# Kernel tuning notes

Measured on AMD Instinct MI355X. Metric: run time of the kernel, lower is better.

Reference implementation:

```python
import jax, jax.numpy as jnp
import numpy as np

EPS = 1e-12  # torch F.normalize eps

def _l2n(x, axis):
    n = jnp.linalg.norm(x, axis=axis, keepdims=True)
    return x / jnp.maximum(n, EPS)

def setup_inputs() -> dict:
    key = jax.random.key(0)
    ks = jax.random.split(key, 11)
    B, N, D = 8, 4096, 512
    s = 1.0 / np.sqrt(D)
    return {
        'a': jax.random.normal(ks[0], (B, N, D), jnp.float32),
        'b': jax.random.normal(ks[1], (B, N, D), jnp.float32),
        'Wq': jax.random.normal(ks[2], (D, D), jnp.float32) * s,
        'bq': jax.random.normal(ks[3], (D,), jnp.float32) * s,
        'Wk': jax.random.normal(ks[4], (D, D), jnp.float32) * s,
        'bk': jax.random.normal(ks[5], (D,), jnp.float32) * s,
        'w_g': jax.random.normal(ks[6], (D, 1), jnp.float32),
        'Wp': jax.random.normal(ks[7], (D, D), jnp.float32) * s,
        'bp': jax.random.normal(ks[8], (D,), jnp.float32) * s,
        'Wf': jax.random.normal(ks[9], (D, D), jnp.float32) * s,
        'bf': jax.random.normal(ks[10], (D,), jnp.float32) * s,
    }

def reference(a, b, Wq, bq, Wk, bk, w_g, Wp, bp, Wf, bf):
    D = a.shape[-1]
    scale = D ** (-0.5)
    query = _l2n(jnp.einsum('bnd,ed->bne', a, Wq) + bq, axis=-1)   # [B,N,D]
    key = _l2n(jnp.einsum('bnd,ed->bne', b, Wk) + bk, axis=-1)     # [B,N,D]
    A = (query @ w_g) * scale                                      # [B,N,1]
    A = _l2n(A, axis=1)                                            # normalize over seq
    G = jnp.sum(A * query, axis=1)                                 # [B,D] learned pooling
    gk = G[:, None, :] * key                                       # broadcast [B,N,D]
    out = jnp.einsum('bnd,ed->bne', gk, Wp) + bp + query           # residual
    out = jnp.einsum('bnd,ed->bne', out, Wf) + bf
    return out
```

## Files before the change

### kernel.cpp

```cpp
#include <hip/hip_runtime.h>
#include <stdint.h>

#define DD 512
#define MTOT 32768

typedef float f32x4 __attribute__((ext_vector_type(4)));
typedef __bf16 bf16x8 __attribute__((ext_vector_type(8)));

static __device__ __forceinline__ unsigned short f2bf(float f) {
  union { float f; unsigned int u; } c; c.f = f;
  unsigned int r = c.u + 0x7fffu + ((c.u >> 16) & 1u);
  return (unsigned short)(r >> 16);
}
static __device__ __forceinline__ float bf2f(unsigned short h) {
  union { unsigned int u; float f; } c; c.u = ((unsigned int)h) << 16;
  return c.f;
}

union FragU { uint4 u; bf16x8 b; };

static __device__ __forceinline__ void load_lds16(const void* g, void* l) {
  __builtin_amdgcn_global_load_lds(
      (const __attribute__((address_space(1))) void*)g,
      (__attribute__((address_space(3))) void*)l, 16, 0, 0);
}

__global__ __launch_bounds__(256) void cvt_k(const float* __restrict__ src,
                                             unsigned short* __restrict__ dst) {
  int i = (blockIdx.x * 256 + threadIdx.x) * 4;
  float4 f = *(const float4*)(src + i);
  ushort4 h;
  h.x = f2bf(f.x); h.y = f2bf(f.y); h.z = f2bf(f.z); h.w = f2bf(f.w);
  *(ushort4*)(dst + i) = h;
}

__global__ __launch_bounds__(256) void cvt3w_k(const float* __restrict__ W0,
    const float* __restrict__ W1, const float* __restrict__ W2,
    unsigned short* __restrict__ D0, unsigned short* __restrict__ D1,
    unsigned short* __restrict__ D2) {
  int slab = blockIdx.x >> 8;
  int off = ((blockIdx.x & 255) * 256 + threadIdx.x) * 4;
  const float* s = slab == 0 ? W0 : slab == 1 ? W1 : W2;
  unsigned short* d = slab == 0 ? D0 : slab == 1 ? D1 : D2;
  float4 f = *(const float4*)(s + off);
  ushort4 h;
  h.x = f2bf(f.x); h.y = f2bf(f.y); h.z = f2bf(f.z); h.w = f2bf(f.w);
  *(ushort4*)(d + off) = h;
}

__global__ __launch_bounds__(256) void scalew_k(const float* __restrict__ Wp,
    const float* __restrict__ G, unsigned short* __restrict__ out) {
  int i = (blockIdx.x * 256 + threadIdx.x) * 4;
  int b = i >> 18;
  int rem = i & 262143;
  int d = rem & 511;
  float4 w = *(const float4*)(Wp + rem);
  float4 g = *(const float4*)(G + b * DD + d);
  ushort4 h;
  h.x = f2bf(w.x * g.x); h.y = f2bf(w.y * g.y);
  h.z = f2bf(w.z * g.z); h.w = f2bf(w.w * g.w);
  *(ushort4*)(out + i) = h;
}

template<int BBATCH, int EMODE>
__global__ __launch_bounds__(256) void gemm_k(
    const unsigned short* __restrict__ X,
    const unsigned short* __restrict__ Wb,
    const float* __restrict__ bias,
    const unsigned short* __restrict__ Qadd,
    void* __restrict__ Cv) {
  __shared__ unsigned short As[128 * 64];
  __shared__ unsigned short Bs[128 * 64];
  const int tid = threadIdx.x;
  const int lane = tid & 63, wave = tid >> 6;
  const int row0 = blockIdx.x * 128, col0 = blockIdx.y * 128;
  const unsigned short* W = Wb + (BBATCH ? (size_t)(row0 >> 12) * 262144 : 0);

  const int sr = lane >> 3;
  const int scol = ((lane & 7) ^ sr) * 8;
  const unsigned short* Ag = X + (size_t)(row0 + wave * 32 + sr) * DD + scol;
  const unsigned short* Bg = W + (size_t)(col0 + wave * 32 + sr) * DD + scol;
  const int ldsb = wave * 32 * 64;

  const int fr = lane & 15, quad = lane >> 4;
  const int wr = (wave >> 1) * 64, wc = (wave & 1) * 64;
  const int sw0 = ((quad ^ (fr & 7)) * 8);
  const int sw1 = (((quad + 4) ^ (fr & 7)) * 8);

  f32x4 acc[4][4] = {};

  for (int k0 = 0; k0 < DD; k0 += 64) {
#pragma unroll
    for (int q = 0; q < 4; q++) {
      load_lds16(Ag + (size_t)q * 8 * DD + k0, As + ldsb + q * 8 * 64);
      load_lds16(Bg + (size_t)q * 8 * DD + k0, Bs + ldsb + q * 8 * 64);
    }
    __syncthreads();
#pragma unroll
    for (int kk = 0; kk < 2; kk++) {
      const int sw = kk ? sw1 : sw0;
      bf16x8 af[4], bfr[4];
#pragma unroll
      for (int i = 0; i < 4; i++) {
        FragU u; u.u = *(const uint4*)&As[(wr + i * 16 + fr) * 64 + sw];
        af[i] = u.b;
      }
#pragma unroll
      for (int j = 0; j < 4; j++) {
        FragU u; u.u = *(const uint4*)&Bs[(wc + j * 16 + fr) * 64 + sw];
        bfr[j] = u.b;
      }
#pragma unroll
      for (int i = 0; i < 4; i++)
#pragma unroll
        for (int j = 0; j < 4; j++)
          acc[i][j] = __builtin_amdgcn_mfma_f32_16x16x32_bf16(af[i], bfr[j], acc[i][j], 0, 0, 0);
    }
    __syncthreads();
  }
#pragma unroll
  for (int j = 0; j < 4; j++) {
    int gc = col0 + wc + j * 16 + fr;
    float bv = bias[gc];
#pragma unroll
    for (int i = 0; i < 4; i++) {
      int gr0 = row0 + wr + i * 16 + quad * 4;
#pragma unroll
      for (int r = 0; r < 4; r++) {
        size_t idx = (size_t)(gr0 + r) * DD + gc;
        float v = acc[i][j][r] + bv;
        if (EMODE == 1) v += bf2f(Qadd[idx]);
        if (EMODE <= 1) ((unsigned short*)Cv)[idx] = f2bf(v);
        else            ((float*)Cv)[idx] = v;
      }
    }
  }
}

__global__ __launch_bounds__(256) void norm_k(unsigned short* __restrict__ Q,
    unsigned short* __restrict__ K, const float* __restrict__ wg,
    float* __restrict__ Araw) {
  const int lane = threadIdx.x & 63, wave = threadIdx.x >> 6;
  const size_t row = (size_t)blockIdx.x * 4 + wave;
  unsigned short* p = (blockIdx.y == 0 ? Q : K) + row * DD + lane * 8;
  uint4 u = *(uint4*)p;
  unsigned short* hp = (unsigned short*)&u;
  float v[8];
  float ss = 0.f;
#pragma unroll
  for (int t = 0; t < 8; t++) { v[t] = bf2f(hp[t]); ss += v[t] * v[t]; }
#pragma unroll
  for (int m = 1; m < 64; m <<= 1) ss += __shfl_xor(ss, m, 64);
  float inv = 1.0f / fmaxf(sqrtf(ss), 1e-12f);
#pragma unroll
  for (int t = 0; t < 8; t++) { v[t] *= inv; hp[t] = f2bf(v[t]); }
  *(uint4*)p = u;
  if (blockIdx.y == 0) {
    const float4* wp = (const float4*)(wg + lane * 8);
    float4 w0 = wp[0], w1 = wp[1];
    float dot = v[0] * w0.x + v[1] * w0.y + v[2] * w0.z + v[3] * w0.w +
                v[4] * w1.x + v[5] * w1.y + v[6] * w1.z + v[7] * w1.w;
#pragma unroll
    for (int m = 1; m < 64; m <<= 1) dot += __shfl_xor(dot, m, 64);
    if (lane == 0) Araw[row] = dot;
  }
}

__global__ __launch_bounds__(512) void reduce_s_k(const float* __restrict__ Araw,
    float* __restrict__ sinv, float* __restrict__ G) {
  const int b = blockIdx.x, t = threadIdx.x;
  G[b * DD + t] = 0.f;
  float ss = 0.f;
  for (int i = t; i < 4096; i += 512) { float v = Araw[b * 4096 + i]; ss += v * v; }
#pragma unroll
  for (int m = 1; m < 64; m <<= 1) ss += __shfl_xor(ss, m, 64);
  __shared__ float sred[8];
  if ((t & 63) == 0) sred[t >> 6] = ss;
  __syncthreads();
  if (t == 0) {
    float tot = 0.f;
    for (int i = 0; i < 8; i++) tot += sred[i];
    sinv[b] = 1.0f / fmaxf(sqrtf(tot), 1e-12f);
  }
}

__global__ __launch_bounds__(256) void pool_k(const float* __restrict__ Araw,
    const float* __restrict__ sinv, const unsigned short* __restrict__ Q,
    float* __restrict__ G) {
  const int b = blockIdx.x >> 5;
  const int chunk = blockIdx.x & 31;
  const int rbase = b * 4096 + chunk * 128;
  const float si = sinv[b];
  const int t = threadIdx.x;
  float a0 = 0.f, a1 = 0.f;
  for (int r = 0; r < 128; r++) {
    float w = Araw[rbase + r] * si;
    const unsigned short* qr = Q + (size_t)(rbase + r) * DD;
    a0 += w * bf2f(qr[t]);
    a1 += w * bf2f(qr[t + 256]);
  }
  atomicAdd(&G[b * DD + t], a0);
  atomicAdd(&G[b * DD + t + 256], a1);
}

extern "C" void kernel_launch(void* const* d_in, const int* in_sizes, int n_in,
                              void* d_out, int out_size, void* d_ws, size_t ws_size,
                              hipStream_t stream) {
  const float* a   = (const float*)d_in[0];
  const float* b   = (const float*)d_in[1];
  const float* Wq  = (const float*)d_in[2];
  const float* bq  = (const float*)d_in[3];
  const float* Wk  = (const float*)d_in[4];
  const float* bk  = (const float*)d_in[5];
  const float* wg  = (const float*)d_in[6];
  const float* Wp  = (const float*)d_in[7];
  const float* bp  = (const float*)d_in[8];
  const float* Wf  = (const float*)d_in[9];
  const float* bfb = (const float*)d_in[10];

  const size_t WELEM = 262144;
  const size_t MD = (size_t)MTOT * DD;

  unsigned short* ABb = (unsigned short*)d_ws;
  unsigned short* Qb  = ABb + MD;
  unsigned short* Kb  = Qb + MD;
  unsigned short* Wqb = Kb + MD;
  unsigned short* Wkb = Wqb + WELEM;
  unsigned short* Wfb = Wkb + WELEM;
  unsigned short* Wps = Wfb + WELEM;
  float* Araw = (float*)(Wps + 8 * WELEM);
  float* sinv = Araw + MTOT;
  float* G    = sinv + 64;

  cvt_k<<<dim3(16384), dim3(256), 0, stream>>>(a, ABb);
  cvt3w_k<<<dim3(768), dim3(256), 0, stream>>>(Wq, Wk, Wf, Wqb, Wkb, Wfb);
  gemm_k<0, 0><<<dim3(256, 4), dim3(256), 0, stream>>>(ABb, Wqb, bq, nullptr, Qb);
  cvt_k<<<dim3(16384), dim3(256), 0, stream>>>(b, ABb);
  gemm_k<0, 0><<<dim3(256, 4), dim3(256), 0, stream>>>(ABb, Wkb, bk, nullptr, Kb);
  norm_k<<<dim3(MTOT / 4, 2), dim3(256), 0, stream>>>(Qb, Kb, wg, Araw);
  reduce_s_k<<<dim3(8), dim3(512), 0, stream>>>(Araw, sinv, G);
  pool_k<<<dim3(256), dim3(256), 0, stream>>>(Araw, sinv, Qb, G);
  scalew_k<<<dim3(2048), dim3(256), 0, stream>>>(Wp, G, Wps);
  gemm_k<1, 1><<<dim3(256, 4), dim3(256), 0, stream>>>(Kb, Wps, bp, Qb, ABb);
  gemm_k<0, 2><<<dim3(256, 4), dim3(256), 0, stream>>>(ABb, Wfb, bfb, nullptr, d_out);
}
```

Before: 330.6 us.

## Fuse row L2 norms into GEMM epilogues and batch Q/K projections

Removes the separate norm pass by computing per-row sum-of-squares and the w_g dot product inside the Q/K GEMM epilogue with shuffles and atomics. Normalization is deferred: Q and K stay unnormalized in bf16, and the reciprocal norms are applied as row scales in the later GEMM epilogue and in the pooling weights. The a/b conversions and the Q/K GEMMs are each merged into one launch, and the stats buffer is zeroed inside the weight-prep kernel. This saves a full read-modify-write of Q and K, at the cost of atomic traffic and slightly different bf16 rounding, because the unnormalized values are stored.

```diff
diff --git a/kernel.cpp b/kernel.cpp
--- a/kernel.cpp
+++ b/kernel.cpp
@@ -3,6 +3,8 @@
 
 #define DD 512
 #define MTOT 32768
+#define MD ((size_t)MTOT * DD)
+#define WELEM 262144
 
 typedef float f32x4 __attribute__((ext_vector_type(4)));
 typedef __bf16 bf16x8 __attribute__((ext_vector_type(8)));
@@ -25,34 +27,41 @@
       (__attribute__((address_space(3))) void*)l, 16, 0, 0);
 }
 
-__global__ __launch_bounds__(256) void cvt_k(const float* __restrict__ src,
-                                             unsigned short* __restrict__ dst) {
-  int i = (blockIdx.x * 256 + threadIdx.x) * 4;
-  float4 f = *(const float4*)(src + i);
+__global__ __launch_bounds__(256) void cvt2_k(const float* __restrict__ a,
+    const float* __restrict__ b, unsigned short* __restrict__ dst) {
+  int i = blockIdx.x * 1024 + threadIdx.x * 4;
+  const float* src = (i < (int)MD) ? (a + i) : (b + (i - (int)MD));
+  float4 f = *(const float4*)src;
   ushort4 h;
   h.x = f2bf(f.x); h.y = f2bf(f.y); h.z = f2bf(f.z); h.w = f2bf(f.w);
   *(ushort4*)(dst + i) = h;
 }
 
-__global__ __launch_bounds__(256) void cvt3w_k(const float* __restrict__ W0,
-    const float* __restrict__ W1, const float* __restrict__ W2,
-    unsigned short* __restrict__ D0, unsigned short* __restrict__ D1,
-    unsigned short* __restrict__ D2) {
-  int slab = blockIdx.x >> 8;
-  int off = ((blockIdx.x & 255) * 256 + threadIdx.x) * 4;
-  const float* s = slab == 0 ? W0 : slab == 1 ? W1 : W2;
-  unsigned short* d = slab == 0 ? D0 : slab == 1 ? D1 : D2;
-  float4 f = *(const float4*)(s + off);
-  ushort4 h;
-  h.x = f2bf(f.x); h.y = f2bf(f.y); h.z = f2bf(f.z); h.w = f2bf(f.w);
-  *(ushort4*)(d + off) = h;
+__global__ __launch_bounds__(256) void prep_k(const float* __restrict__ Wq,
+    const float* __restrict__ Wk, const float* __restrict__ Wf,
+    unsigned short* __restrict__ Wqkb, unsigned short* __restrict__ Wfb,
+    float* __restrict__ stats) {
+  if (blockIdx.x < 768) {
+    int slab = blockIdx.x >> 8;
+    int off = (blockIdx.x & 255) * 1024 + threadIdx.x * 4;
+    const float* s = slab == 0 ? Wq : slab == 1 ? Wk : Wf;
+    unsigned short* d = slab == 0 ? Wqkb : slab == 1 ? (Wqkb + WELEM) : Wfb;
+    float4 f = *(const float4*)(s + off);
+    ushort4 h;
+    h.x = f2bf(f.x); h.y = f2bf(f.y); h.z = f2bf(f.z); h.w = f2bf(f.w);
+    *(ushort4*)(d + off) = h;
+  } else {
+    int off = (blockIdx.x - 768) * 1024 + threadIdx.x * 4;
+    float4 z = {0.f, 0.f, 0.f, 0.f};
+    *(float4*)(stats + off) = z;
+  }
 }
 
 __global__ __launch_bounds__(256) void scalew_k(const float* __restrict__ Wp,
     const float* __restrict__ G, unsigned short* __restrict__ out) {
-  int i = (blockIdx.x * 256 + threadIdx.x) * 4;
+  int i = blockIdx.x * 1024 + threadIdx.x * 4;
   int b = i >> 18;
-  int rem = i & 262143;
+  int rem = i & (WELEM - 1);
   int d = rem & 511;
   float4 w = *(const float4*)(Wp + rem);
   float4 g = *(const float4*)(G + b * DD + d);
@@ -62,33 +71,22 @@
   *(ushort4*)(out + i) = h;
 }
 
-template<int BBATCH, int EMODE>
-__global__ __launch_bounds__(256) void gemm_k(
-    const unsigned short* __restrict__ X,
-    const unsigned short* __restrict__ Wb,
-    const float* __restrict__ bias,
-    const unsigned short* __restrict__ Qadd,
-    void* __restrict__ Cv) {
-  __shared__ unsigned short As[128 * 64];
-  __shared__ unsigned short Bs[128 * 64];
+static __device__ __forceinline__ void gemm_main(
+    const unsigned short* __restrict__ X, const unsigned short* __restrict__ W,
+    unsigned short* As, unsigned short* Bs, int row0, int col0,
+    f32x4 acc[4][4]) {
   const int tid = threadIdx.x;
   const int lane = tid & 63, wave = tid >> 6;
-  const int row0 = blockIdx.x * 128, col0 = blockIdx.y * 128;
-  const unsigned short* W = Wb + (BBATCH ? (size_t)(row0 >> 12) * 262144 : 0);
-
   const int sr = lane >> 3;
   const int scol = ((lane & 7) ^ sr) * 8;
   const unsigned short* Ag = X + (size_t)(row0 + wave * 32 + sr) * DD + scol;
   const unsigned short* Bg = W + (size_t)(col0 + wave * 32 + sr) * DD + scol;
   const int ldsb = wave * 32 * 64;
-
   const int fr = lane & 15, quad = lane >> 4;
   const int wr = (wave >> 1) * 64, wc = (wave & 1) * 64;
   const int sw0 = ((quad ^ (fr & 7)) * 8);
   const int sw1 = (((quad + 4) ^ (fr & 7)) * 8);
 
-  f32x4 acc[4][4] = {};
-
   for (int k0 = 0; k0 < DD; k0 += 64) {
 #pragma unroll
     for (int q = 0; q < 4; q++) {
@@ -118,73 +116,97 @@
     }
     __syncthreads();
   }
+}
+
+__global__ __launch_bounds__(256) void gemm_qk_k(
+    const unsigned short* __restrict__ Xab,
+    const unsigned short* __restrict__ Wqk,
+    const float* __restrict__ bq, const float* __restrict__ bk,
+    const float* __restrict__ wg,
+    unsigned short* __restrict__ QK,
+    float* __restrict__ SS, float* __restrict__ Adot) {
+  __shared__ unsigned short As[128 * 64];
+  __shared__ unsigned short Bs[128 * 64];
+  const int z = blockIdx.z;
+  const unsigned short* X = Xab + (size_t)z * MD;
+  const unsigned short* W = Wqk + (size_t)z * WELEM;
+  const float* bias = z ? bk : bq;
+  unsigned short* out = QK + (size_t)z * MD;
+  float* SSp = SS + (size_t)z * MTOT;
+  const int row0 = blockIdx.x * 128, col0 = blockIdx.y * 128;
+
+  f32x4 acc[4][4] = {};
+  gemm_main(X, W, As, Bs, row0, col0, acc);
+
+  const int lane = threadIdx.x & 63, wave = threadIdx.x >> 6;
+  const int fr = lane & 15, quad = lane >> 4;
+  const int wr = (wave >> 1) * 64, wc = (wave & 1) * 64;
+  float ssv[4][4] = {};
+  float dtv[4][4] = {};
 #pragma unroll
   for (int j = 0; j < 4; j++) {
     int gc = col0 + wc + j * 16 + fr;
     float bv = bias[gc];
+    float wgv = (z == 0) ? wg[gc] : 0.f;
 #pragma unroll
     for (int i = 0; i < 4; i++) {
       int gr0 = row0 + wr + i * 16 + quad * 4;
 #pragma unroll
       for (int r = 0; r < 4; r++) {
-        size_t idx = (size_t)(gr0 + r) * DD + gc;
         float v = acc[i][j][r] + bv;
-        if (EMODE == 1) v += bf2f(Qadd[idx]);
-        if (EMODE <= 1) ((unsigned short*)Cv)[idx] = f2bf(v);
-        else            ((float*)Cv)[idx] = v;
-      }
-    }
-  }
-}
-
-__global__ __launch_bounds__(256) void norm_k(unsigned short* __restrict__ Q,
-    unsigned short* __restrict__ K, const float* __restrict__ wg,
-    float* __restrict__ Araw) {
-  const int lane = threadIdx.x & 63, wave = threadIdx.x >> 6;
-  const size_t row = (size_t)blockIdx.x * 4 + wave;
-  unsigned short* p = (blockIdx.y == 0 ? Q : K) + row * DD + lane * 8;
-  uint4 u = *(uint4*)p;
-  unsigned short* hp = (unsigned short*)&u;
-  float v[8];
-  float ss = 0.f;
-#pragma unroll
-  for (int t = 0; t < 8; t++) { v[t] = bf2f(hp[t]); ss += v[t] * v[t]; }
-#pragma unroll
-  for (int m = 1; m < 64; m <<= 1) ss += __shfl_xor(ss, m, 64);
-  float inv = 1.0f / fmaxf(sqrtf(ss), 1e-12f);
-#pragma unroll
-  for (int t = 0; t < 8; t++) { v[t] *= inv; hp[t] = f2bf(v[t]); }
-  *(uint4*)p = u;
-  if (blockIdx.y == 0) {
-    const float4* wp = (const float4*)(wg + lane * 8);
-    float4 w0 = wp[0], w1 = wp[1];
-    float dot = v[0] * w0.x + v[1] * w0.y + v[2] * w0.z + v[3] * w0.w +
-                v[4] * w1.x + v[5] * w1.y + v[6] * w1.z + v[7] * w1.w;
-#pragma unroll
-    for (int m = 1; m < 64; m <<= 1) dot += __shfl_xor(dot, m, 64);
-    if (lane == 0) Araw[row] = dot;
-  }
-}
-
-__global__ __launch_bounds__(512) void reduce_s_k(const float* __restrict__ Araw,
+        out[(size_t)(gr0 + r) * DD + gc] = f2bf(v);
+        ssv[i][r] += v * v;
+        dtv[i][r] += v * wgv;
+      }
+    }
+  }
+#pragma unroll
+  for (int i = 0; i < 4; i++)
+#pragma unroll
+    for (int r = 0; r < 4; r++) {
+      float s = ssv[i][r];
+#pragma unroll
+      for (int m = 1; m < 16; m <<= 1) s += __shfl_xor(s, m, 64);
+      if (z == 0) {
+        float d = dtv[i][r];
+#pragma unroll
+        for (int m = 1; m < 16; m <<= 1) d += __shfl_xor(d, m, 64);
+        if (fr == 0) atomicAdd(&Adot[row0 + wr + i * 16 + quad * 4 + r], d);
+      }
+      if (fr == 0) atomicAdd(&SSp[row0 + wr + i * 16 + quad * 4 + r], s);
+    }
+}
+
+__global__ __launch_bounds__(1024) void reduce2_k(const float* __restrict__ SSQK,
+    const float* __restrict__ Adot, float* __restrict__ rnQ,
+    float* __restrict__ rnK, float* __restrict__ wrow,
     float* __restrict__ sinv, float* __restrict__ G) {
   const int b = blockIdx.x, t = threadIdx.x;
-  G[b * DD + t] = 0.f;
+  if (t < DD) G[b * DD + t] = 0.f;
   float ss = 0.f;
-  for (int i = t; i < 4096; i += 512) { float v = Araw[b * 4096 + i]; ss += v * v; }
+  for (int i = t; i < 4096; i += 1024) {
+    int n = b * 4096 + i;
+    float sq = SSQK[n], sk = SSQK[MTOT + n], ad = Adot[n];
+    float rq = 1.0f / fmaxf(sqrtf(sq), 1e-12f);
+    rnQ[n] = rq;
+    rnK[n] = 1.0f / fmaxf(sqrtf(sk), 1e-12f);
+    wrow[n] = ad / fmaxf(sq, 1e-24f);
+    float araw = ad * rq;
+    ss += araw * araw;
+  }
 #pragma unroll
   for (int m = 1; m < 64; m <<= 1) ss += __shfl_xor(ss, m, 64);
-  __shared__ float sred[8];
+  __shared__ float sred[16];
   if ((t & 63) == 0) sred[t >> 6] = ss;
   __syncthreads();
   if (t == 0) {
     float tot = 0.f;
-    for (int i = 0; i < 8; i++) tot += sred[i];
+    for (int i = 0; i < 16; i++) tot += sred[i];
     sinv[b] = 1.0f / fmaxf(sqrtf(tot), 1e-12f);
   }
 }
 
-__global__ __launch_bounds__(256) void pool_k(const float* __restrict__ Araw,
+__global__ __launch_bounds__(256) void pool_k(const float* __restrict__ wrow,
     const float* __restrict__ sinv, const unsigned short* __restrict__ Q,
     float* __restrict__ G) {
   const int b = blockIdx.x >> 5;
@@ -193,14 +215,83 @@
   const float si = sinv[b];
   const int t = threadIdx.x;
   float a0 = 0.f, a1 = 0.f;
+#pragma unroll 4
   for (int r = 0; r < 128; r++) {
-    float w = Araw[rbase + r] * si;
-    const unsigned short* qr = Q + (size_t)(rbase + r) * DD;
-    a0 += w * bf2f(qr[t]);
-    a1 += w * bf2f(qr[t + 256]);
-  }
-  atomicAdd(&G[b * DD + t], a0);
-  atomicAdd(&G[b * DD + t + 256], a1);
+    float w = wrow[rbase + r] * si;
+    unsigned int q = *(const unsigned int*)(Q + (size_t)(rbase + r) * DD + 2 * t);
+    a0 += w * bf2f((unsigned short)(q & 0xffff));
+    a1 += w * bf2f((unsigned short)(q >> 16));
+  }
+  atomicAdd(&G[b * DD + 2 * t], a0);
+  atomicAdd(&G[b * DD + 2 * t + 1], a1);
+}
+
+__global__ __launch_bounds__(256) void gemm3_k(
+    const unsigned short* __restrict__ K,
+    const unsigned short* __restrict__ Wps,
+    const float* __restrict__ bp,
+    const unsigned short* __restrict__ Qraw,
+    const float* __restrict__ rnK, const float* __restrict__ rnQ,
+    unsigned short* __restrict__ O1) {
+  __shared__ unsigned short As[128 * 64];
+  __shared__ unsigned short Bs[128 * 64];
+  const int row0 = blockIdx.x * 128, col0 = blockIdx.y * 128;
+  const unsigned short* W = Wps + (size_t)(row0 >> 12) * WELEM;
+  f32x4 acc[4][4] = {};
+  gemm_main(K, W, As, Bs, row0, col0, acc);
+  const int lane = threadIdx.x & 63, wave = threadIdx.x >> 6;
+  const int fr = lane & 15, quad = lane >> 4;
+  const int wr = (wave >> 1) * 64, wc = (wave & 1) * 64;
+  float rk[4][4], rq[4][4];
+#pragma unroll
+  for (int i = 0; i < 4; i++)
+#pragma unroll
+    for (int r = 0; r < 4; r++) {
+      int row = row0 + wr + i * 16 + quad * 4 + r;
+      rk[i][r] = rnK[row];
+      rq[i][r] = rnQ[row];
+    }
+#pragma unroll
+  for (int j = 0; j < 4; j++) {
+    int gc = col0 + wc + j * 16 + fr;
+    float bv = bp[gc];
+#pragma unroll
+    for (int i = 0; i < 4; i++) {
+      int gr0 = row0 + wr + i * 16 + quad * 4;
+#pragma unroll
+      for (int r = 0; r < 4; r++) {
+        size_t idx = (size_t)(gr0 + r) * DD + gc;
+        float v = rk[i][r] * acc[i][j][r] + bv + rq[i][r] * bf2f(Qraw[idx]);
+        O1[idx] = f2bf(v);
+      }
+    }
+  }
+}
+
+__global__ __launch_bounds__(256) void gemm4_k(
+    const unsigned short* __restrict__ X,
+    const unsigned short* __restrict__ Wf,
+    const float* __restrict__ bfb, float* __restrict__ out) {
+  __shared__ unsigned short As[128 * 64];
+  __shared__ unsigned short Bs[128 * 64];
+  const int row0 = blockIdx.x * 128, col0 = blockIdx.y * 128;
+  f32x4 acc[4][4] = {};
+  gemm_main(X, Wf, As, Bs, row0, col0, acc);
+  const int lane = threadIdx.x & 63, wave = threadIdx.x >> 6;
+  const int fr = lane & 15, quad = lane >> 4;
+  const int wr = (wave >> 1) * 64, wc = (wave & 1) * 64;
+#pragma unroll
+  for (int j = 0; j < 4; j++) {
+    int gc = col0 + wc + j * 16 + fr;
+    float bv = bfb[gc];
+#pragma unroll
+    for (int i = 0; i < 4; i++) {
+      int gr0 = row0 + wr + i * 16 + quad * 4;
+#pragma unroll
+      for (int r = 0; r < 4; r++)
+        out[(size_t)(gr0 + r) * DD + gc] = acc[i][j][r] + bv;
+    }
+  }
 }
 
 extern "C" void kernel_launch(void* const* d_in, const int* in_sizes, int n_in,
@@ -218,29 +309,26 @@
   const float* Wf  = (const float*)d_in[9];
   const float* bfb = (const float*)d_in[10];
 
-  const size_t WELEM = 262144;
-  const size_t MD = (size_t)MTOT * DD;
-
-  unsigned short* ABb = (unsigned short*)d_ws;
-  unsigned short* Qb  = ABb + MD;
-  unsigned short* Kb  = Qb + MD;
-  unsigned short* Wqb = Kb + MD;
-  unsigned short* Wkb = Wqb + WELEM;
-  unsigned short* Wfb = Wkb + WELEM;
-  unsigned short* Wps = Wfb + WELEM;
-  float* Araw = (float*)(Wps + 8 * WELEM);
-  float* sinv = Araw + MTOT;
+  unsigned short* ABab = (unsigned short*)d_ws;
+  unsigned short* QK   = ABab + 2 * MD;
+  unsigned short* Wqkb = QK + 2 * MD;
+  unsigned short* Wfb  = Wqkb + 2 * WELEM;
+  unsigned short* Wps  = Wfb + WELEM;
+  float* SSQK = (float*)(Wps + 8 * WELEM);
+  float* Adot = SSQK + 2 * MTOT;
+  float* rnQ  = Adot + MTOT;
+  float* rnK  = rnQ + MTOT;
+  float* wrow = rnK + MTOT;
+  float* sinv = wrow + MTOT;
   float* G    = sinv + 64;
 
-  cvt_k<<<dim3(16384), dim3(256), 0, stream>>>(a, ABb);
-  cvt3w_k<<<dim3(768), dim3(256), 0, stream>>>(Wq, Wk, Wf, Wqb, Wkb, Wfb);
-  gemm_k<0, 0><<<dim3(256, 4), dim3(256), 0, stream>>>(ABb, Wqb, bq, nullptr, Qb);
-  cvt_k<<<dim3(16384), dim3(256), 0, stream>>>(b, ABb);
-  gemm_k<0, 0><<<dim3(256, 4), dim3(256), 0, stream>>>(ABb, Wkb, bk, nullptr, Kb);
-  norm_k<<<dim3(MTOT / 4, 2), dim3(256), 0, stream>>>(Qb, Kb, wg, Araw);
-  reduce_s_k<<<dim3(8), dim3(512), 0, stream>>>(Araw, sinv, G);
-  pool_k<<<dim3(256), dim3(256), 0, stream>>>(Araw, sinv, Qb, G);
+  cvt2_k<<<dim3(32768), dim3(256), 0, stream>>>(a, b, ABab);
+  prep_k<<<dim3(864), dim3(256), 0, stream>>>(Wq, Wk, Wf, Wqkb, Wfb, SSQK);
+  gemm_qk_k<<<dim3(256, 4, 2), dim3(256), 0, stream>>>(ABab, Wqkb, bq, bk, wg,
+                                                       QK, SSQK, Adot);
+  reduce2_k<<<dim3(8), dim3(1024), 0, stream>>>(SSQK, Adot, rnQ, rnK, wrow, sinv, G);
+  pool_k<<<dim3(256), dim3(256), 0, stream>>>(wrow, sinv, QK, G);
   scalew_k<<<dim3(2048), dim3(256), 0, stream>>>(Wp, G, Wps);
-  gemm_k<1, 1><<<dim3(256, 4), dim3(256), 0, stream>>>(Kb, Wps, bp, Qb, ABb);
-  gemm_k<0, 2><<<dim3(256, 4), dim3(256), 0, stream>>>(ABb, Wfb, bfb, nullptr, d_out);
-}
+  gemm3_k<<<dim3(256, 4), dim3(256), 0, stream>>>(QK + MD, Wps, bp, QK, rnK, rnQ, ABab);
+  gemm4_k<<<dim3(256, 4), dim3(256), 0, stream>>>(ABab, Wfb, bfb, (float*)d_out);
+}
```

After: 338.7 us. 1.02x slower.
